# Optimization experiments

Measured on AMD Instinct MI355X. Metric: run time of the kernel, lower is better.

The kernel has to match this reference:

```python
import jax, jax.numpy as jnp
import numpy as np

N_HEAD = 2


def _time_encode(ts, freq, phase):
    # ts [N, L] -> [N, L, time_dim]; harmonic = cos(ts * basis_freq + phase)
    return jnp.cos(ts[..., None] * freq + phase)


def _layer_norm(x, g, b, eps=1e-5):
    m = jnp.mean(x, axis=-1, keepdims=True)
    v = jnp.mean((x - m) ** 2, axis=-1, keepdims=True)
    return (x - m) / jnp.sqrt(v + eps) * g + b


def _attn(src, src_t, ngh, ngh_t, mask, wq, wk, wv, fcw, fcb, lng, lnb, m1w, m1b, m2w, m2b):
    # TGAT AttnModel: src [N,h], src_t [N,1,h], ngh [N,K,h], ngh_t [N,K,h], mask [N,K] bool
    q = jnp.concatenate([src[:, None, :], src_t], axis=-1)  # [N,1,D], D=2h
    k = jnp.concatenate([ngh, ngh_t], axis=-1)              # [N,K,D]
    N, K, D = k.shape
    dk = D // N_HEAD
    qh = (q @ wq.T).reshape(N, 1, N_HEAD, dk)
    kh = (k @ wk.T).reshape(N, K, N_HEAD, dk)
    vh = (k @ wv.T).reshape(N, K, N_HEAD, dk)
    scores = jnp.einsum('nqhd,nkhd->nhqk', qh, kh) / jnp.sqrt(jnp.float32(dk))
    scores = jnp.where(mask[:, None, None, :], jnp.float32(-1e10), scores)
    a = jax.nn.softmax(scores, axis=-1)
    out = jnp.einsum('nhqk,nkhd->nqhd', a, vh).reshape(N, 1, D)
    out = out @ fcw.T + fcb
    out = _layer_norm(out + q, lng, lnb)[:, 0, :]  # residual + LN, squeeze query dim
    # MergeLayer: fc2(relu(fc1(cat[out, src])))
    h = jax.nn.relu(jnp.concatenate([out, src], axis=-1) @ m1w.T + m1b)
    return h @ m2w.T + m2b


def setup_inputs() -> dict:
    key = jax.random.key(0)
    ks = jax.random.split(key, 20)
    B, K, F, H = 2048, 20, 128, 128
    D, L, NAE, NNODE = 2 * H, 2, 4096, 100000
    s = 0.05
    n = lambda i, shape, sc=1.0: jax.random.normal(ks[i], shape, dtype=jnp.float32) * sc
    inp = {}
    inp['src_feat'] = n(0, (B, F))
    inp['src_t'] = jax.random.uniform(ks[1], (B,), jnp.float32, 0.0, 1000.0)
    inp['ngh1_idx'] = jax.random.randint(ks[2], (B, K), 0, NNODE)
    inp['ngh1_t'] = jax.random.uniform(ks[3], (B, K), jnp.float32, 0.0, 1000.0)
    inp['ngh1_feat'] = n(4, (B, K, F))
    inp['ngh2_idx'] = jax.random.randint(ks[5], (B * K, K), 0, NNODE)
    inp['ngh2_t'] = jax.random.uniform(ks[6], (B * K, K), jnp.float32, 0.0, 1000.0)
    inp['ngh2_feat'] = n(7, (B * K, K, F))
    inp['ae_x'] = n(8, (NAE, H))
    inp['ae_adj'] = jax.random.uniform(ks[9], (NAE, NAE), jnp.float32)
    inp['W_lin'] = n(10, (H, F), s)
    inp['b_lin'] = jnp.zeros((H,), jnp.float32)
    inp['basis_freq'] = (1.0 / 10 ** jnp.linspace(0.0, 9.0, H)).astype(jnp.float32)
    inp['phase'] = jnp.zeros((H,), jnp.float32)
    inp['attn_wq'] = n(11, (L, D, D), s)
    inp['attn_wk'] = n(12, (L, D, D), s)
    inp['attn_wv'] = n(13, (L, D, D), s)
    inp['attn_fc_w'] = n(14, (L, D, D), s)
    inp['attn_fc_b'] = jnp.zeros((L, D), jnp.float32)
    inp['attn_ln_g'] = jnp.ones((L, D), jnp.float32)
    inp['attn_ln_b'] = jnp.zeros((L, D), jnp.float32)
    inp['mrg_fc1_w'] = n(15, (L, H, D + H), s)
    inp['mrg_fc1_b'] = jnp.zeros((L, H), jnp.float32)
    inp['mrg_fc2_w'] = n(16, (L, H, H), s)
    inp['mrg_fc2_b'] = jnp.zeros((L, H), jnp.float32)
    inp['W_gc'] = n(17, (H, H), s)
    inp['b_gc'] = jnp.zeros((H,), jnp.float32)
    return inp


def reference(src_feat, src_t, ngh1_idx, ngh1_t, ngh1_feat, ngh2_idx, ngh2_t, ngh2_feat,
              ae_x, ae_adj, W_lin, b_lin, basis_freq, phase,
              attn_wq, attn_wk, attn_wv, attn_fc_w, attn_fc_b, attn_ln_g, attn_ln_b,
              mrg_fc1_w, mrg_fc1_b, mrg_fc2_w, mrg_fc2_b, W_gc, b_gc):
    B, K = ngh1_idx.shape
    BK = B * K
    lin = lambda x: x @ W_lin.T + b_lin
    te = lambda ts: _time_encode(ts, basis_freq, phase)
    ap = lambda i: (attn_wq[i], attn_wk[i], attn_wv[i], attn_fc_w[i], attn_fc_b[i],
                    attn_ln_g[i], attn_ln_b[i], mrg_fc1_w[i], mrg_fc1_b[i],
                    mrg_fc2_w[i], mrg_fc2_b[i])
    mask1 = ngh1_idx == 0
    mask2 = ngh2_idx == 0
    t0_B = te(jnp.zeros((B, 1), jnp.float32))
    t0_BK = te(jnp.zeros((BK, 1), jnp.float32))
    t1 = te(src_t[:, None] - ngh1_t)                         # [B,K,H]
    t2 = te(ngh1_t.reshape(BK)[:, None] - ngh2_t)            # [BK,K,H]
    # tem_conv(curr=2): layer-1 embeddings of src and its neighbors (attn layer 0)
    src_l1 = _attn(lin(src_feat), t0_B, lin(ngh1_feat), t1, mask1, *ap(0))    # [B,H]
    ngh_l1 = _attn(lin(ngh1_feat.reshape(BK, -1)), t0_BK, lin(ngh2_feat), t2, mask2, *ap(0))
    ngh_l1 = ngh_l1.reshape(B, K, -1)
    # top-level attention (attn layer 1)
    src_embed = _attn(src_l1, t0_B, ngh_l1, t1, mask1, *ap(1))                # [B,H]
    # GNN_SnapAuto autoencoder: GraphConvolution + sigmoid decode + MSE
    gc_z = ae_adj @ (ae_x @ W_gc) + b_gc
    recon_loss = jnp.mean((ae_adj - jax.nn.sigmoid(gc_z @ gc_z.T)) ** 2)
    return src_embed, recon_loss
```

## Files before the change

### kernel.cpp

```cpp
#include <hip/hip_runtime.h>
#include <math.h>


typedef _Float16 h2 __attribute__((ext_vector_type(2)));
typedef _Float16 h4 __attribute__((ext_vector_type(4)));
typedef _Float16 h8 __attribute__((ext_vector_type(8)));
typedef float f4 __attribute__((ext_vector_type(4)));


__global__ __launch_bounds__(256) void k_prep_a(
    const float* __restrict__ phase, const float* __restrict__ wq,
    const float* __restrict__ wk, const float* __restrict__ wvw,
    const float* __restrict__ Wlin, const float* __restrict__ blin,
    const float* __restrict__ m1w, const float* __restrict__ m2w,
    const float* __restrict__ Wgc,
    float* __restrict__ te0, float* __restrict__ cbf, float* __restrict__ Mb,
    float* __restrict__ OWa,
    _Float16* __restrict__ Wlinh, _Float16* __restrict__ m1wh,
    _Float16* __restrict__ m2wh, _Float16* __restrict__ WgcTh,
    float* __restrict__ lacc)
{
  __shared__ float te[128];
  __shared__ float bqv[128];
  int b = blockIdx.x, tid = threadIdx.x;

  if (b < 4) {
    int l = b >> 1, h = b & 1;
    if (tid < 128) {
      te[tid] = cosf(phase[tid]);
      if (b == 0) te0[tid] = te[tid];
    }
    __syncthreads();
    if (tid < 128) {
      const float* wr = wq + ((size_t)(l * 256 + h * 128 + tid)) * 256 + 128;
      float s = 0.f;
      for (int k = 0; k < 128; k++) s += wr[k] * te[k];
      bqv[tid] = s;
    }
    __syncthreads();
    {
      const float* wkb = wk + (size_t)l * 65536 + (size_t)h * 32768;
      float s = 0.f;
      for (int d = 0; d < 128; d++) s += wkb[(size_t)d * 256 + tid] * bqv[d];
      cbf[(l * 2 + h) * 256 + tid] = s;
    }
    return;
  }
  b -= 4;
  if (b < 512) {
    int lh = b >> 7, bx = b & 127;
    int l = lh >> 1, h = lh & 1;
    int idx = bx * 256 + tid;
    int e = idx >> 7, s = idx & 127;
    const float* wkb = wk + (size_t)l * 65536 + (size_t)h * 32768;
    const float* wqb = wq + (size_t)l * 65536 + (size_t)h * 32768;
    float acc = 0.f;
    for (int d = 0; d < 128; d++)
      acc += wkb[(size_t)d * 256 + e] * wqb[(size_t)d * 256 + s];
    Mb[(size_t)lh * 32768 + idx] = acc;
    return;
  }
  b -= 512;
  if (b < 780) {
    int ci = b / 260, bx = b % 260;
    int lyr = (ci == 2) ? 1 : 0;
    int ul  = (ci == 0) ? 1 : 0;
    float* OW = OWa + (size_t)ci * 2 * 128 * 260;
    const float* wvl = wvw + (size_t)lyr * 65536;
    int idx = bx * 256 + tid;
    int u = idx % 260; int d = (idx / 260) % 128; int h = idx / (260 * 128);
    const float* wr = wvl + (size_t)(h * 128 + d) * 256;
    float val = 0.f;
    if (u < 128) {
      if (ul) { for (int cc = 0; cc < 128; cc++) val += wr[cc] * Wlin[cc * 128 + u]; }
      else val = wr[u];
    } else if (u < 256) {
      val = wr[u];
    } else if (u == 256) {
      if (ul) { for (int cc = 0; cc < 128; cc++) val += wr[cc] * blin[cc]; }
    }
    OW[idx] = val;
    return;
  }
  b -= 780;
  {
    int idx = b * 256 + tid;
    if (idx == 0) lacc[0] = 0.f;
    int i = idx;
    if (i < 16384) { Wlinh[i] = (_Float16)Wlin[i]; return; }
    i -= 16384;
    if (i < 98304) { m1wh[i] = (_Float16)m1w[i]; return; }
    i -= 98304;
    if (i < 32768) { m2wh[i] = (_Float16)m2w[i]; return; }
    i -= 32768;
    {
      int c = i >> 7, r = i & 127;
      WgcTh[i] = (_Float16)Wgc[(size_t)r * 128 + c];
    }
  }
}


__global__ __launch_bounds__(256) void k_prep_b(
    const float* __restrict__ Mb, const float* __restrict__ cbf,
    const float* __restrict__ Wlin, const float* __restrict__ blin,
    const float* __restrict__ fcw, const float* __restrict__ OWa,
    _Float16* __restrict__ SWa, float* __restrict__ cba,
    _Float16* __restrict__ Fa)
{
  int b = blockIdx.x, tid = threadIdx.x;
  if (b < 780) {
    int ci = b / 260, bx = b % 260;
    int lyr = (ci == 2) ? 1 : 0;
    int ul  = (ci == 0) ? 1 : 0;
    const float* M2 = Mb + (size_t)lyr * 2 * 32768;
    const float* c2 = cbf + (size_t)lyr * 512;
    _Float16* SW = SWa + (size_t)ci * 520 * 128;
    float* cb = cba + (size_t)ci * 520;
    int idx = bx * 256 + tid;
    int urow = idx / 128, s = idx % 128;
    int h = urow / 260, u = urow % 260;
    const float* M = M2 + (size_t)h * 32768;
    const float* c = c2 + h * 256;
    float val = 0.f, cbv = 0.f;
    if (u < 128) {
      if (ul) {
        for (int cc = 0; cc < 128; cc++) {
          float w = Wlin[cc * 128 + u];
          val += w * M[cc * 128 + s];
          cbv += w * c[cc];
        }
      } else { val = M[u * 128 + s]; cbv = c[u]; }
    } else if (u < 256) {
      val = M[u * 128 + s]; cbv = c[u];
    } else if (u == 256) {
      if (ul) {
        for (int cc = 0; cc < 128; cc++) {
          float w = blin[cc];
          val += w * M[cc * 128 + s];
          cbv += w * c[cc];
        }
      }
    }
    SW[(size_t)urow * 128 + s] = (_Float16)val;
    if (s == 0) cb[urow] = cbv;
    return;
  }
  b -= 780;
  {
    int yy = b / 260, bx = b % 260;
    int ci = yy >> 1, h = yy & 1;
    int lyr = (ci == 2) ? 1 : 0;
    int idx = bx * 256 + tid;
    int p = idx / 260, u = idx % 260;
    const float* fw = fcw + (size_t)lyr * 65536 + (size_t)p * 256 + h * 128;
    const float* ow = OWa + (size_t)ci * 2 * 128 * 260 + (size_t)h * 128 * 260;
    float s = 0.f;
    for (int d = 0; d < 128; d++) s += fw[d] * ow[(size_t)d * 260 + u];
    Fa[(size_t)ci * 256 * 520 + (size_t)p * 520 + h * 260 + u] = (_Float16)s;
  }
}


struct GemmJob {
  const float* A; const _Float16* B; const float* bias; float* C;
  int lda, ldb, ldc, M, N, K, cmode, klen, gx, gy, nblk;
};

__device__ __forceinline__ void gemm128_body(int lb, const GemmJob& g) {
  __shared__ _Float16 As[128][72];
  __shared__ _Float16 Bs[128][72];
  int bx = lb % g.gx;
  int rest = lb / g.gx;
  int by = rest % g.gy;
  int z = rest / g.gy;

  int tid = threadIdx.x;
  int wv = tid >> 6, lane = tid & 63;
  int wm = wv >> 1, wn = wv & 1;
  int row0 = bx * 128, col0 = by * 128;
  int m0 = wm * 64, n0 = wn * 64;
  int lr = lane & 15, lk = lane >> 4;
  int kbeg = z * g.klen;
  int kend = kbeg + g.klen; if (kend > g.K) kend = g.K;

  f4 acc[4][4];
#pragma unroll
  for (int i = 0; i < 4; i++)
#pragma unroll
    for (int j = 0; j < 4; j++) acc[i][j] = (f4)0.f;

  int arow = tid >> 1;
  int acol = (tid & 1) * 32;
  int gar = row0 + arow;
  int gbr = col0 + arow;
  bool bvalid = gbr < g.N;

  for (int k0 = kbeg; k0 < kend; k0 += 64) {
    __syncthreads();
#pragma unroll
    for (int j = 0; j < 8; j++) {
      int ka = k0 + acol + j * 4;
      f4 v = (f4)0.f;
      if (ka < g.K) v = *(const f4*)&g.A[(size_t)gar * g.lda + ka];
      h4 hv = { (_Float16)v.x, (_Float16)v.y, (_Float16)v.z, (_Float16)v.w };
      *(h4*)&As[arow][acol + j * 4] = hv;
    }
#pragma unroll
    for (int j = 0; j < 8; j++) {
      int ka = k0 + acol + j * 4;
      h4 hv = (h4)(_Float16)0.f;
      if (bvalid && ka < g.K) hv = *(const h4*)&g.B[(size_t)gbr * g.ldb + ka];
      *(h4*)&Bs[arow][acol + j * 4] = hv;
    }
    __syncthreads();
#pragma unroll
    for (int kk = 0; kk < 2; kk++) {
      h8 af[4], bf[4];
#pragma unroll
      for (int i = 0; i < 4; i++)
        af[i] = *(h8*)&As[m0 + i * 16 + lr][kk * 32 + lk * 8];
#pragma unroll
      for (int j = 0; j < 4; j++)
        bf[j] = *(h8*)&Bs[n0 + j * 16 + lr][kk * 32 + lk * 8];
#pragma unroll
      for (int i = 0; i < 4; i++)
#pragma unroll
        for (int j = 0; j < 4; j++)
          acc[i][j] = __builtin_amdgcn_mfma_f32_16x16x32_f16(af[i], bf[j], acc[i][j], 0, 0, 0);
    }
  }
  float* Cz = g.C + (size_t)z * g.M * g.ldc;
#pragma unroll
  for (int j = 0; j < 4; j++) {
    int c = col0 + n0 + j * 16 + lr;
    if (c >= g.N) continue;
    float bz = (g.bias && z == 0) ? g.bias[c] : 0.f;
#pragma unroll
    for (int i = 0; i < 4; i++) {
      int rbase = row0 + m0 + i * 16 + lk * 4;
#pragma unroll
      for (int r = 0; r < 4; r++) {
        int rr = rbase + r;
        float v = acc[i][j][r] + bz;
        if (g.cmode == 0) Cz[(size_t)rr * g.ldc + c] = v;
        else if (g.cmode == 1) ((_Float16*)g.C)[(size_t)rr * g.ldc + c] = (_Float16)v;
        else ((_Float16*)g.C)[(size_t)c * g.ldc + rr] = (_Float16)v;
      }
    }
  }
}

__global__ __launch_bounds__(256) void k_gemm_multi(
    GemmJob ja, GemmJob jb, GemmJob jc, const float* lacc, float* finout)
{
  int b = blockIdx.x;
  if (b < ja.nblk) { gemm128_body(b, ja); return; }
  b -= ja.nblk;
  if (b < jb.nblk) { gemm128_body(b, jb); return; }
  b -= jb.nblk;
  if (b < jc.nblk) { gemm128_body(b, jc); return; }
  if (finout && threadIdx.x == 0)
    finout[0] = lacc[0] * (1.0f / (4096.0f * 4096.0f));
}


struct ScoreJob {
  _Float16* UY; const float* feat; const float* tsrc; const float* tngh;
  const int* idx; int rows;
};

__device__ void score_body(int row, const ScoreJob& J,
                           const float* __restrict__ freq,
                           const float* __restrict__ phase)
{
  __shared__ _Float16 fsh[20][136];
  __shared__ _Float16 tesh[20][136];
  __shared__ _Float16 ush[544];
  __shared__ float ssh[2][20];
  __shared__ float ash[2][20];
  __shared__ float dtsh[20];
  __shared__ int   msh[20];
  int tid = threadIdx.x;
  _Float16* UY = J.UY;

  if (tid < 20) {
    dtsh[tid] = J.tsrc[row] - J.tngh[(size_t)row * 20 + tid];
    msh[tid] = (J.idx[(size_t)row * 20 + tid] == 0);
  }
  if (tid < 130) {
    h4 v = *(const h4*)&UY[(size_t)row * 520 + tid * 4];
    int p4 = (tid < 65) ? tid : tid + 1;
    *(h4*)&ush[p4 * 4] = v;
  }
  const float4* fg = (const float4*)(J.feat + (size_t)row * 2560);
  for (int i = tid; i < 640; i += 256) {
    int j = i >> 5, c4 = i & 31;
    float4 v = fg[i];
    h4 hv = { (_Float16)v.x, (_Float16)v.y, (_Float16)v.z, (_Float16)v.w };
    *(h4*)&fsh[j][c4 * 4] = hv;
  }
  __syncthreads();
  for (int i = tid; i < 2560; i += 256) {
    int j = i >> 7, t = i & 127;
    tesh[j][t] = (_Float16)__cosf(dtsh[j] * freq[t] + phase[t]);
  }
  __syncthreads();

  int g = tid >> 4, li = tid & 15;
#pragma unroll
  for (int it = 0; it < 3; it++) {
    int t = it * 16 + g;
    int valid = (t < 40);
    int h = valid ? (t / 20) : 0;
    int j = valid ? (t % 20) : 0;
    float part = 0.f;
    if (valid) {
      const _Float16* xp = (li < 8) ? &fsh[j][li * 16] : &tesh[j][(li - 8) * 16];
      const _Float16* up = &ush[h * 264 + li * 16];
#pragma unroll
      for (int e = 0; e < 8; e++) {
        h2 a = *(const h2*)(xp + e * 2);
        h2 b = *(const h2*)(up + e * 2);
        part = __builtin_amdgcn_fdot2(a, b, part, false);
      }
    }
    for (int m = 8; m; m >>= 1) part += __shfl_xor(part, m, 16);
    if (valid && li == 0) ssh[h][j] = part + (float)ush[h * 264 + 256];
  }
  __syncthreads();

  if (tid < 64) {
    int head = tid >> 5, l2 = tid & 31;
    const float scale = 0.08838834764831845f;
    float s = (l2 < 20) ? (msh[l2] ? -1e10f : ssh[head][l2] * scale) : -3.0e38f;
    float mx = s;
    for (int m = 16; m; m >>= 1) mx = fmaxf(mx, __shfl_xor(mx, m, 32));
    float e = (l2 < 20) ? __expf(s - mx) : 0.f;
    float sum = e;
    for (int m = 16; m; m >>= 1) sum += __shfl_xor(sum, m, 32);
    if (l2 < 20) ash[head][l2] = e / sum;
  }
  __syncthreads();

  {
    int p = tid;
    const _Float16* colp = (p < 128) ? &fsh[0][p] : &tesh[0][p - 128];
    float a0 = 0.f, a1 = 0.f;
#pragma unroll 5
    for (int j = 0; j < 20; j++) {
      float x = (float)colp[j * 136];
      a0 += ash[0][j] * x;
      a1 += ash[1][j] * x;
    }
    UY[(size_t)row * 520 + p] = (_Float16)a0;
    UY[(size_t)row * 520 + 260 + p] = (_Float16)a1;
  }
  if (tid < 8) {
    int p = (tid < 4) ? (256 + tid) : (512 + tid);
    _Float16 v = (_Float16)((tid == 0 || tid == 4) ? 1.f : 0.f);
    UY[(size_t)row * 520 + p] = v;
  }
}

__global__ __launch_bounds__(256, 8) void k_score_multi(
    ScoreJob ja, ScoreJob jb, const float* __restrict__ freq,
    const float* __restrict__ phase,
    const float* __restrict__ zp, _Float16* __restrict__ zh, int nzb)
{
  int b = blockIdx.x;
  if (b < ja.rows) { score_body(b, ja, freq, phase); return; }
  b -= ja.rows;
  if (b < jb.rows) { score_body(b, jb, freq, phase); return; }
  b -= jb.rows;
  if (b < nzb) {
    int i = b * 256 + threadIdx.x;
    const f4* zp4 = (const f4*)zp;
    f4 s = (f4)0.f;
#pragma unroll
    for (int p = 0; p < 8; p++) {
      f4 v = zp4[(size_t)p * 131072 + i];
      s.x += v.x; s.y += v.y; s.z += v.z; s.w += v.w;
    }
    h4 o = { (_Float16)s.x, (_Float16)s.y, (_Float16)s.z, (_Float16)s.w };
    ((h4*)zh)[i] = o;
  }
}


struct TailJob {
  const _Float16* U; const _Float16* F; const float* fcb; const float* srcv;
  const float* lng; const float* lnb;
  const _Float16* m1w; const float* m1b;
  const _Float16* m2w; const float* m2b;
  float* outp; int nblk;
};

__device__ void tail_body(int blk, const TailJob& J, const float* __restrict__ te0)
{
  __shared__ _Float16 Ps[64][264];
  __shared__ _Float16 Ss[64][136];
  __shared__ float redS[64][4], redQ[64][4];
  __shared__ float mrow[64], rrow[64];
  int tid = threadIdx.x;
  int wv = tid >> 6, lane = tid & 63;
  int lr = lane & 15, lk = lane >> 4;
  int row0 = blk * 64;
  int n0 = wv * 64;

  {
    const float4* sg = (const float4*)(J.srcv + (size_t)row0 * 128);
    for (int i = tid; i < 2048; i += 256) {
      int rr = i >> 5, c4 = i & 31;
      float4 v = sg[i];
      h4 hv = { (_Float16)v.x, (_Float16)v.y, (_Float16)v.z, (_Float16)v.w };
      *(h4*)&Ss[rr][c4 * 4] = hv;
    }
  }

  f4 acc[4][4];
#pragma unroll
  for (int i = 0; i < 4; i++)
#pragma unroll
    for (int j = 0; j < 4; j++) acc[i][j] = (f4)0.f;
  for (int kt = 0; kt < 17; kt++) {
    int kb = kt * 32 + lk * 8;
    bool ok = (kb + 8 <= 520);
    h8 af[4], bf[4];
#pragma unroll
    for (int i = 0; i < 4; i++)
      af[i] = ok ? *(const h8*)&J.U[(size_t)(row0 + i * 16 + lr) * 520 + kb]
                 : (h8)(_Float16)0.f;
#pragma unroll
    for (int j = 0; j < 4; j++)
      bf[j] = ok ? *(const h8*)&J.F[(size_t)(n0 + j * 16 + lr) * 520 + kb]
                 : (h8)(_Float16)0.f;
#pragma unroll
    for (int i = 0; i < 4; i++)
#pragma unroll
      for (int j = 0; j < 4; j++)
        acc[i][j] = __builtin_amdgcn_mfma_f32_16x16x32_f16(af[i], bf[j], acc[i][j], 0, 0, 0);
  }

#pragma unroll
  for (int i = 0; i < 4; i++) {
#pragma unroll
    for (int r = 0; r < 4; r++) {
      int row_l = i * 16 + lk * 4 + r;
      float rs = 0.f, rq = 0.f;
#pragma unroll
      for (int j = 0; j < 4; j++) {
        int c = n0 + j * 16 + lr;
        float q = (c < 128) ? J.srcv[(size_t)(row0 + row_l) * 128 + c] : te0[c - 128];
        float v = acc[i][j][r] + J.fcb[c] + q;
        acc[i][j][r] = v;
        rs += v; rq += v * v;
      }
      for (int m = 8; m; m >>= 1) {
        rs += __shfl_xor(rs, m, 16);
        rq += __shfl_xor(rq, m, 16);
      }
      if (lr == 0) { redS[row_l][wv] = rs; redQ[row_l][wv] = rq; }
    }
  }
  __syncthreads();
  if (tid < 64) {
    float s4 = redS[tid][0] + redS[tid][1] + redS[tid][2] + redS[tid][3];
    float q4 = redQ[tid][0] + redQ[tid][1] + redQ[tid][2] + redQ[tid][3];
    float mean = s4 * (1.0f / 256.0f);
    float var = q4 * (1.0f / 256.0f) - mean * mean;
    mrow[tid] = mean;
    rrow[tid] = rsqrtf(var + 1e-5f);
  }
  __syncthreads();
#pragma unroll
  for (int i = 0; i < 4; i++) {
#pragma unroll
    for (int r = 0; r < 4; r++) {
      int row_l = i * 16 + lk * 4 + r;
      float mean = mrow[row_l], rstd = rrow[row_l];
#pragma unroll
      for (int j = 0; j < 4; j++) {
        int c = n0 + j * 16 + lr;
        Ps[row_l][c] = (_Float16)((acc[i][j][r] - mean) * rstd * J.lng[c] + J.lnb[c]);
      }
    }
  }
  __syncthreads();

  int wm = wv >> 1, wn = wv & 1;
  f4 a2[2][4];
#pragma unroll
  for (int i = 0; i < 2; i++)
#pragma unroll
    for (int j = 0; j < 4; j++) a2[i][j] = (f4)0.f;
  for (int kk = 0; kk < 12; kk++) {
    int kb = kk * 32 + lk * 8;
    h8 af[2], bf[4];
#pragma unroll
    for (int i = 0; i < 2; i++) {
      int rl = wm * 32 + i * 16 + lr;
      af[i] = (kb < 256) ? *(const h8*)&Ps[rl][kb] : *(const h8*)&Ss[rl][kb - 256];
    }
#pragma unroll
    for (int j = 0; j < 4; j++)
      bf[j] = *(const h8*)&J.m1w[(size_t)(wn * 64 + j * 16 + lr) * 384 + kb];
#pragma unroll
    for (int i = 0; i < 2; i++)
#pragma unroll
      for (int j = 0; j < 4; j++)
        a2[i][j] = __builtin_amdgcn_mfma_f32_16x16x32_f16(af[i], bf[j], a2[i][j], 0, 0, 0);
  }
  __syncthreads();
#pragma unroll
  for (int i = 0; i < 2; i++) {
#pragma unroll
    for (int j = 0; j < 4; j++) {
      int c = wn * 64 + j * 16 + lr;
      float bz = J.m1b[c];
#pragma unroll
      for (int r = 0; r < 4; r++) {
        float v = a2[i][j][r] + bz;
        if (v < 0.f) v = 0.f;
        Ss[wm * 32 + i * 16 + lk * 4 + r][c] = (_Float16)v;
      }
    }
  }
  __syncthreads();

  f4 a3[2][4];
#pragma unroll
  for (int i = 0; i < 2; i++)
#pragma unroll
    for (int j = 0; j < 4; j++) a3[i][j] = (f4)0.f;
#pragma unroll
  for (int kk = 0; kk < 4; kk++) {
    int kb = kk * 32 + lk * 8;
    h8 af[2], bf[4];
#pragma unroll
    for (int i = 0; i < 2; i++)
      af[i] = *(const h8*)&Ss[wm * 32 + i * 16 + lr][kb];
#pragma unroll
    for (int j = 0; j < 4; j++)
      bf[j] = *(const h8*)&J.m2w[(size_t)(wn * 64 + j * 16 + lr) * 128 + kb];
#pragma unroll
    for (int i = 0; i < 2; i++)
#pragma unroll
      for (int j = 0; j < 4; j++)
        a3[i][j] = __builtin_amdgcn_mfma_f32_16x16x32_f16(af[i], bf[j], a3[i][j], 0, 0, 0);
  }
#pragma unroll
  for (int j = 0; j < 4; j++) {
    int c = wn * 64 + j * 16 + lr;
    float bz = J.m2b[c];
#pragma unroll
    for (int i = 0; i < 2; i++) {
#pragma unroll
      for (int r = 0; r < 4; r++) {
        int rl = wm * 32 + i * 16 + lk * 4 + r;
        J.outp[(size_t)(row0 + rl) * 128 + c] = a3[i][j][r] + bz;
      }
    }
  }
}

__device__ void loss_body(int b, const _Float16* __restrict__ z,
                          const float* __restrict__ adj, float* __restrict__ acc)
{
  int bi = b & 31, bj = b >> 5;
  int tid = threadIdx.x;
  int wv = tid >> 6, lane = tid & 63;
  int wm = wv >> 1, wn = wv & 1;
  int lr = lane & 15, lk = lane >> 4;
  int row0 = bi * 128 + wm * 64;
  int col0 = bj * 128 + wn * 64;

  f4 accf[4][4];
#pragma unroll
  for (int i = 0; i < 4; i++)
#pragma unroll
    for (int j = 0; j < 4; j++) accf[i][j] = (f4)0.f;

#pragma unroll
  for (int kk = 0; kk < 4; kk++) {
    int ko = kk * 32 + lk * 8;
    h8 af[4], bf[4];
#pragma unroll
    for (int i = 0; i < 4; i++)
      af[i] = *(const h8*)&z[(size_t)(row0 + i * 16 + lr) * 128 + ko];
#pragma unroll
    for (int j = 0; j < 4; j++)
      bf[j] = *(const h8*)&z[(size_t)(col0 + j * 16 + lr) * 128 + ko];
#pragma unroll
    for (int i = 0; i < 4; i++)
#pragma unroll
      for (int j = 0; j < 4; j++)
        accf[i][j] = __builtin_amdgcn_mfma_f32_16x16x32_f16(af[i], bf[j], accf[i][j], 0, 0, 0);
  }

  float lsum = 0.f;
#pragma unroll
  for (int i = 0; i < 4; i++) {
    int rbase = row0 + i * 16 + lk * 4;
#pragma unroll
    for (int r = 0; r < 4; r++) {
      const float* arow = adj + (size_t)(rbase + r) * 4096;
#pragma unroll
      for (int j = 0; j < 4; j++) {
        float x = accf[i][j][r];
        float s = 1.0f / (1.0f + __expf(-x));
        float d = arow[col0 + j * 16 + lr] - s;
        lsum += d * d;
      }
    }
  }
  for (int m = 32; m; m >>= 1) lsum += __shfl_xor(lsum, m, 64);
  if (lane == 0) atomicAdd(acc, lsum);
}

__global__ __launch_bounds__(256) void k_tail_loss(
    TailJob ja, TailJob jb, const float* __restrict__ te0,
    const _Float16* __restrict__ z, const float* __restrict__ adj,
    float* __restrict__ lacc, int nloss)
{
  int b = blockIdx.x;
  if (b < ja.nblk) { tail_body(b, ja, te0); return; }
  b -= ja.nblk;
  if (b < jb.nblk) { tail_body(b, jb, te0); return; }
  b -= jb.nblk;
  if (b < nloss) loss_body(b, z, adj, lacc);
}


extern "C" void kernel_launch(void* const* d_in, const int* in_sizes, int n_in,
                              void* d_out, int out_size, void* d_ws, size_t ws_size,
                              hipStream_t stream) {
  const float* src_feat  = (const float*)d_in[0];
  const float* src_t     = (const float*)d_in[1];
  const int*   ngh1_idx  = (const int*)d_in[2];
  const float* ngh1_t    = (const float*)d_in[3];
  const float* ngh1_feat = (const float*)d_in[4];
  const int*   ngh2_idx  = (const int*)d_in[5];
  const float* ngh2_t    = (const float*)d_in[6];
  const float* ngh2_feat = (const float*)d_in[7];
  const float* ae_x      = (const float*)d_in[8];
  const float* ae_adj    = (const float*)d_in[9];
  const float* W_lin     = (const float*)d_in[10];
  const float* b_lin     = (const float*)d_in[11];
  const float* freq      = (const float*)d_in[12];
  const float* phase     = (const float*)d_in[13];
  const float* wq        = (const float*)d_in[14];
  const float* wk        = (const float*)d_in[15];
  const float* wvp       = (const float*)d_in[16];
  const float* fcw       = (const float*)d_in[17];
  const float* fcb       = (const float*)d_in[18];
  const float* lng       = (const float*)d_in[19];
  const float* lnb       = (const float*)d_in[20];
  const float* m1w       = (const float*)d_in[21];
  const float* m1b       = (const float*)d_in[22];
  const float* m2w       = (const float*)d_in[23];
  const float* m2b       = (const float*)d_in[24];
  const float* W_gc      = (const float*)d_in[25];
  const float* b_gc      = (const float*)d_in[26];
  float* out = (float*)d_out;

  const int NB = 2048, NA = 40960;

  char* w = (char*)d_ws;
  size_t off = 0;
  auto alloc = [&](size_t bytes) -> void* {
    void* p = (void*)(w + off);
    off += (bytes + 255) & ~(size_t)255;
    return p;
  };
  float* te0    = (float*)alloc(128 * 4);
  float* linS   = (float*)alloc((size_t)NB * 128 * 4);
  float* lin1   = (float*)alloc((size_t)NA * 128 * 4);
  float* src_l1 = (float*)alloc((size_t)NB * 128 * 4);
  float* ngh_l1 = (float*)alloc((size_t)NA * 128 * 4);
  float* Mb     = (float*)alloc((size_t)4 * 32768 * 4);
  float* cbf    = (float*)alloc(4 * 256 * 4);
  _Float16* SWh = (_Float16*)alloc((size_t)3 * 520 * 128 * 2);
  float* cbU    = (float*)alloc(3 * 520 * 4);
  float* OW     = (float*)alloc((size_t)3 * 2 * 128 * 260 * 4);
  _Float16* Fh  = (_Float16*)alloc((size_t)3 * 256 * 520 * 2);
  _Float16* Wlinh = (_Float16*)alloc(16384 * 2);
  _Float16* m1wh  = (_Float16*)alloc((size_t)2 * 128 * 384 * 2);
  _Float16* m2wh  = (_Float16*)alloc((size_t)2 * 128 * 128 * 2);
  _Float16* WgcTh = (_Float16*)alloc(16384 * 2);
  _Float16* xwTh  = (_Float16*)alloc((size_t)4096 * 128 * 2);
  float* zpart    = (float*)alloc((size_t)8 * 4096 * 128 * 4);
  _Float16* zh    = (_Float16*)alloc((size_t)4096 * 128 * 2);
  float* lacc     = (float*)alloc(256);
  _Float16* UbufA = (_Float16*)alloc((size_t)NA * 520 * 2);
  _Float16* UbufB = (_Float16*)alloc((size_t)NB * 520 * 2);
  _Float16* UbufC = (_Float16*)alloc((size_t)NB * 520 * 2);

  k_prep_a<<<1936, 256, 0, stream>>>(phase, wq, wk, wvp, W_lin, b_lin, m1w, m2w,
                                     W_gc, te0, cbf, Mb, OW, Wlinh, m1wh, m2wh,
                                     WgcTh, lacc);
  k_prep_b<<<2340, 256, 0, stream>>>(Mb, cbf, W_lin, b_lin, fcw, OW, SWh, cbU, Fh);

  GemmJob j0 = {};

  GemmJob jLinS = { src_feat,  Wlinh, b_lin,   linS,         128, 128, 128,
                    2048, 128, 128, 0, 128, 16, 1, 16 };
  GemmJob jLin1 = { ngh1_feat, Wlinh, b_lin,   lin1,         128, 128, 128,
                    40960, 128, 128, 0, 128, 320, 1, 320 };
  GemmJob jXwT  = { ae_x,      WgcTh, nullptr, (float*)xwTh, 128, 128, 4096,
                    4096, 128, 128, 2, 128, 32, 1, 32 };
  k_gemm_multi<<<368, 256, 0, stream>>>(jLinS, jLin1, jXwT, nullptr, nullptr);

  GemmJob jUA = { lin1, SWh,              cbU,       (float*)UbufA, 128, 128, 520,
                  40960, 520, 128, 1, 128, 320, 5, 1600 };
  GemmJob jUB = { linS, SWh + 520 * 128,  cbU + 520, (float*)UbufB, 128, 128, 520,
                  2048, 520, 128, 1, 128, 16, 5, 80 };
  GemmJob jZB = { ae_adj, xwTh, b_gc, zpart, 4096, 4096, 128,
                  4096, 128, 4096, 0, 512, 32, 1, 256 };
  k_gemm_multi<<<1936, 256, 0, stream>>>(jUA, jUB, jZB, nullptr, nullptr);

  ScoreJob sA = { UbufA, ngh2_feat, ngh1_t, ngh2_t, ngh2_idx, NA };
  ScoreJob sB = { UbufB, lin1,      src_t,  ngh1_t, ngh1_idx, NB };
  k_score_multi<<<NA + NB + 512, 256, 0, stream>>>(sA, sB, freq, phase,
                                                   zpart, zh, 512);

  TailJob tA = { UbufA, Fh,             fcb, lin1, lng, lnb,
                 m1wh, m1b, m2wh, m2b, ngh_l1, NA / 64 };
  TailJob tB = { UbufB, Fh + 256 * 520, fcb, linS, lng, lnb,
                 m1wh, m1b, m2wh, m2b, src_l1, NB / 64 };
  k_tail_loss<<<NA / 64 + NB / 64 + 1024, 256, 0, stream>>>(
      tA, tB, te0, zh, ae_adj, lacc, 1024);

  GemmJob jUC = { src_l1, SWh + 2 * 520 * 128, cbU + 2 * 520, (float*)UbufC,
                  128, 128, 520, 2048, 520, 128, 1, 128, 16, 5, 80 };
  k_gemm_multi<<<81, 256, 0, stream>>>(jUC, j0, j0, lacc, out + (size_t)NB * 128);

  ScoreJob sC = { UbufC, ngh_l1, src_t, ngh1_t, ngh1_idx, NB };
  ScoreJob s0 = {};
  k_score_multi<<<NB, 256, 0, stream>>>(sC, s0, freq, phase, nullptr, nullptr, 0);

  TailJob tC = { UbufC, Fh + 2 * 256 * 520, fcb + 256, src_l1, lng + 256, lnb + 256,
                 m1wh + 128 * 384, m1b + 128, m2wh + 128 * 128, m2b + 128,
                 out, NB / 64 };
  TailJob t0 = {};
  k_tail_loss<<<NB / 64, 256, 0, stream>>>(tC, t0, te0, nullptr, nullptr,
                                           nullptr, 0);
}
```

Before: 502.1 us.

## Fuse top-level attention stage into one kernel and merge first GEMMs into prep

The three final launches for the top-level attention (U projection GEMM, score/softmax/aggregation, and the fc+LayerNorm+merge MLP tail) are replaced by a single kernel. Each of its 32 blocks handles 64 rows end to end and keeps intermediates in shared memory, so the UbufC round trip and two launch gaps go away. The lin/xwT GEMM jobs are also folded into the k_prep_b launch to drop one more launch. The trade-off is that the fused kernel runs only 32 blocks, one per CU, which may leave most of the GPU idle during that stage.

```diff
diff --git a/kernel.cpp b/kernel.cpp
--- a/kernel.cpp
+++ b/kernel.cpp
@@ -101,12 +101,103 @@
 }
 
 
+struct GemmJob {
+  const float* A; const _Float16* B; const float* bias; float* C;
+  int lda, ldb, ldc, M, N, K, cmode, klen, gx, gy, nblk;
+};
+
+__device__ __forceinline__ void gemm128_body(int lb, const GemmJob& g) {
+  __shared__ _Float16 As[128][72];
+  __shared__ _Float16 Bs[128][72];
+  int bx = lb % g.gx;
+  int rest = lb / g.gx;
+  int by = rest % g.gy;
+  int z = rest / g.gy;
+
+  int tid = threadIdx.x;
+  int wv = tid >> 6, lane = tid & 63;
+  int wm = wv >> 1, wn = wv & 1;
+  int row0 = bx * 128, col0 = by * 128;
+  int m0 = wm * 64, n0 = wn * 64;
+  int lr = lane & 15, lk = lane >> 4;
+  int kbeg = z * g.klen;
+  int kend = kbeg + g.klen; if (kend > g.K) kend = g.K;
+
+  f4 acc[4][4];
+#pragma unroll
+  for (int i = 0; i < 4; i++)
+#pragma unroll
+    for (int j = 0; j < 4; j++) acc[i][j] = (f4)0.f;
+
+  int arow = tid >> 1;
+  int acol = (tid & 1) * 32;
+  int gar = row0 + arow;
+  int gbr = col0 + arow;
+  bool bvalid = gbr < g.N;
+
+  for (int k0 = kbeg; k0 < kend; k0 += 64) {
+    __syncthreads();
+#pragma unroll
+    for (int j = 0; j < 8; j++) {
+      int ka = k0 + acol + j * 4;
+      f4 v = (f4)0.f;
+      if (ka < g.K) v = *(const f4*)&g.A[(size_t)gar * g.lda + ka];
+      h4 hv = { (_Float16)v.x, (_Float16)v.y, (_Float16)v.z, (_Float16)v.w };
+      *(h4*)&As[arow][acol + j * 4] = hv;
+    }
+#pragma unroll
+    for (int j = 0; j < 8; j++) {
+      int ka = k0 + acol + j * 4;
+      h4 hv = (h4)(_Float16)0.f;
+      if (bvalid && ka < g.K) hv = *(const h4*)&g.B[(size_t)gbr * g.ldb + ka];
+      *(h4*)&Bs[arow][acol + j * 4] = hv;
+    }
+    __syncthreads();
+#pragma unroll
+    for (int kk = 0; kk < 2; kk++) {
+      h8 af[4], bf[4];
+#pragma unroll
+      for (int i = 0; i < 4; i++)
+        af[i] = *(h8*)&As[m0 + i * 16 + lr][kk * 32 + lk * 8];
+#pragma unroll
+      for (int j = 0; j < 4; j++)
+        bf[j] = *(h8*)&Bs[n0 + j * 16 + lr][kk * 32 + lk * 8];
+#pragma unroll
+      for (int i = 0; i < 4; i++)
+#pragma unroll
+        for (int j = 0; j < 4; j++)
+          acc[i][j] = __builtin_amdgcn_mfma_f32_16x16x32_f16(af[i], bf[j], acc[i][j], 0, 0, 0);
+    }
+  }
+  float* Cz = g.C + (size_t)z * g.M * g.ldc;
+#pragma unroll
+  for (int j = 0; j < 4; j++) {
+    int c = col0 + n0 + j * 16 + lr;
+    if (c >= g.N) continue;
+    float bz = (g.bias && z == 0) ? g.bias[c] : 0.f;
+#pragma unroll
+    for (int i = 0; i < 4; i++) {
+      int rbase = row0 + m0 + i * 16 + lk * 4;
+#pragma unroll
+      for (int r = 0; r < 4; r++) {
+        int rr = rbase + r;
+        float v = acc[i][j][r] + bz;
+        if (g.cmode == 0) Cz[(size_t)rr * g.ldc + c] = v;
+        else if (g.cmode == 1) ((_Float16*)g.C)[(size_t)rr * g.ldc + c] = (_Float16)v;
+        else ((_Float16*)g.C)[(size_t)c * g.ldc + rr] = (_Float16)v;
+      }
+    }
+  }
+}
+
+
 __global__ __launch_bounds__(256) void k_prep_b(
     const float* __restrict__ Mb, const float* __restrict__ cbf,
     const float* __restrict__ Wlin, const float* __restrict__ blin,
     const float* __restrict__ fcw, const float* __restrict__ OWa,
     _Float16* __restrict__ SWa, float* __restrict__ cba,
-    _Float16* __restrict__ Fa)
+    _Float16* __restrict__ Fa,
+    GemmJob j1, GemmJob j2, GemmJob j3)
 {
   int b = blockIdx.x, tid = threadIdx.x;
   if (b < 780) {
@@ -147,7 +238,7 @@
     return;
   }
   b -= 780;
-  {
+  if (b < 1560) {
     int yy = b / 260, bx = b % 260;
     int ci = yy >> 1, h = yy & 1;
     int lyr = (ci == 2) ? 1 : 0;
@@ -158,101 +249,18 @@
     float s = 0.f;
     for (int d = 0; d < 128; d++) s += fw[d] * ow[(size_t)d * 260 + u];
     Fa[(size_t)ci * 256 * 520 + (size_t)p * 520 + h * 260 + u] = (_Float16)s;
-  }
+    return;
+  }
+  b -= 1560;
+  if (b < j1.nblk) { gemm128_body(b, j1); return; }
+  b -= j1.nblk;
+  if (b < j2.nblk) { gemm128_body(b, j2); return; }
+  b -= j2.nblk;
+  if (b < j3.nblk) { gemm128_body(b, j3); return; }
 }
 
-
-struct GemmJob {
-  const float* A; const _Float16* B; const float* bias; float* C;
-  int lda, ldb, ldc, M, N, K, cmode, klen, gx, gy, nblk;
-};
-
-__device__ __forceinline__ void gemm128_body(int lb, const GemmJob& g) {
-  __shared__ _Float16 As[128][72];
-  __shared__ _Float16 Bs[128][72];
-  int bx = lb % g.gx;
-  int rest = lb / g.gx;
-  int by = rest % g.gy;
-  int z = rest / g.gy;
-
-  int tid = threadIdx.x;
-  int wv = tid >> 6, lane = tid & 63;
-  int wm = wv >> 1, wn = wv & 1;
-  int row0 = bx * 128, col0 = by * 128;
-  int m0 = wm * 64, n0 = wn * 64;
-  int lr = lane & 15, lk = lane >> 4;
-  int kbeg = z * g.klen;
-  int kend = kbeg + g.klen; if (kend > g.K) kend = g.K;
-
-  f4 acc[4][4];
-#pragma unroll
-  for (int i = 0; i < 4; i++)
-#pragma unroll
-    for (int j = 0; j < 4; j++) acc[i][j] = (f4)0.f;
-
-  int arow = tid >> 1;
-  int acol = (tid & 1) * 32;
-  int gar = row0 + arow;
-  int gbr = col0 + arow;
-  bool bvalid = gbr < g.N;
-
-  for (int k0 = kbeg; k0 < kend; k0 += 64) {
-    __syncthreads();
-#pragma unroll
-    for (int j = 0; j < 8; j++) {
-      int ka = k0 + acol + j * 4;
-      f4 v = (f4)0.f;
-      if (ka < g.K) v = *(const f4*)&g.A[(size_t)gar * g.lda + ka];
-      h4 hv = { (_Float16)v.x, (_Float16)v.y, (_Float16)v.z, (_Float16)v.w };
-      *(h4*)&As[arow][acol + j * 4] = hv;
-    }
-#pragma unroll
-    for (int j = 0; j < 8; j++) {
-      int ka = k0 + acol + j * 4;
-      h4 hv = (h4)(_Float16)0.f;
-      if (bvalid && ka < g.K) hv = *(const h4*)&g.B[(size_t)gbr * g.ldb + ka];
-      *(h4*)&Bs[arow][acol + j * 4] = hv;
-    }
-    __syncthreads();
-#pragma unroll
-    for (int kk = 0; kk < 2; kk++) {
-      h8 af[4], bf[4];
-#pragma unroll
-      for (int i = 0; i < 4; i++)
-        af[i] = *(h8*)&As[m0 + i * 16 + lr][kk * 32 + lk * 8];
-#pragma unroll
-      for (int j = 0; j < 4; j++)
-        bf[j] = *(h8*)&Bs[n0 + j * 16 + lr][kk * 32 + lk * 8];
-#pragma unroll
-      for (int i = 0; i < 4; i++)
-#pragma unroll
-        for (int j = 0; j < 4; j++)
-          acc[i][j] = __builtin_amdgcn_mfma_f32_16x16x32_f16(af[i], bf[j], acc[i][j], 0, 0, 0);
-    }
-  }
-  float* Cz = g.C + (size_t)z * g.M * g.ldc;
-#pragma unroll
-  for (int j = 0; j < 4; j++) {
-    int c = col0 + n0 + j * 16 + lr;
-    if (c >= g.N) continue;
-    float bz = (g.bias && z == 0) ? g.bias[c] : 0.f;
-#pragma unroll
-    for (int i = 0; i < 4; i++) {
-      int rbase = row0 + m0 + i * 16 + lk * 4;
-#pragma unroll
-      for (int r = 0; r < 4; r++) {
-        int rr = rbase + r;
-        float v = acc[i][j][r] + bz;
-        if (g.cmode == 0) Cz[(size_t)rr * g.ldc + c] = v;
-        else if (g.cmode == 1) ((_Float16*)g.C)[(size_t)rr * g.ldc + c] = (_Float16)v;
-        else ((_Float16*)g.C)[(size_t)c * g.ldc + rr] = (_Float16)v;
-      }
-    }
-  }
-}
-
 __global__ __launch_bounds__(256) void k_gemm_multi(
-    GemmJob ja, GemmJob jb, GemmJob jc, const float* lacc, float* finout)
+    GemmJob ja, GemmJob jb, GemmJob jc)
 {
   int b = blockIdx.x;
   if (b < ja.nblk) { gemm128_body(b, ja); return; }
@@ -260,8 +268,6 @@
   if (b < jb.nblk) { gemm128_body(b, jb); return; }
   b -= jb.nblk;
   if (b < jc.nblk) { gemm128_body(b, jc); return; }
-  if (finout && threadIdx.x == 0)
-    finout[0] = lacc[0] * (1.0f / (4096.0f * 4096.0f));
 }
 
 
@@ -321,8 +327,8 @@
 #pragma unroll
       for (int e = 0; e < 8; e++) {
         h2 a = *(const h2*)(xp + e * 2);
-        h2 b = *(const h2*)(up + e * 2);
-        part = __builtin_amdgcn_fdot2(a, b, part, false);
+        h2 b2 = *(const h2*)(up + e * 2);
+        part = __builtin_amdgcn_fdot2(a, b2, part, false);
       }
     }
     for (int m = 8; m; m >>= 1) part += __shfl_xor(part, m, 16);
@@ -629,6 +635,333 @@
   if (b < jb.nblk) { tail_body(b, jb, te0); return; }
   b -= jb.nblk;
   if (b < nloss) loss_body(b, z, adj, lacc);
+}
+
+
+__global__ __launch_bounds__(256, 1) void k_callC(
+    const float* __restrict__ src_l1,
+    const _Float16* __restrict__ SWc,
+    const float* __restrict__ cbc,
+    const float* __restrict__ featp,
+    const float* __restrict__ tsrc, const float* __restrict__ tngh,
+    const int* __restrict__ idxp,
+    const float* __restrict__ freq, const float* __restrict__ phase,
+    const _Float16* __restrict__ F,
+    const float* __restrict__ fcb, const float* __restrict__ lng,
+    const float* __restrict__ lnb,
+    const _Float16* __restrict__ m1w, const float* __restrict__ m1b,
+    const _Float16* __restrict__ m2w, const float* __restrict__ m2b,
+    const float* __restrict__ te0,
+    float* __restrict__ outp, const float* __restrict__ lacc,
+    float* __restrict__ finout)
+{
+  __shared__ _Float16 Uls[64][536];
+  __shared__ __align__(16) _Float16 Scr[4][5440];
+  __shared__ _Float16 Ssh[64][136];
+  __shared__ float redS[64][4], redQ[64][4];
+  __shared__ float mrow[64], rrow[64];
+  __shared__ float sshA[4][2][20], ashA[4][2][20], dtA[4][20];
+  __shared__ int   mskA[4][20];
+  __shared__ float fqs[128], phs[128];
+
+  int tid = threadIdx.x;
+  int wv = tid >> 6, lane = tid & 63;
+  int lr = lane & 15, lk = lane >> 4;
+  int row0 = blockIdx.x * 64;
+
+  if (blockIdx.x == 0 && tid == 0)
+    finout[0] = lacc[0] * (1.0f / (4096.0f * 4096.0f));
+  if (tid < 128) { fqs[tid] = freq[tid]; phs[tid] = phase[tid]; }
+
+  {
+    const float4* sg = (const float4*)(src_l1 + (size_t)row0 * 128);
+    for (int i = tid; i < 2048; i += 256) {
+      int rr = i >> 5, c4 = i & 31;
+      float4 v = sg[i];
+      h4 hv = { (_Float16)v.x, (_Float16)v.y, (_Float16)v.z, (_Float16)v.w };
+      *(h4*)&Ssh[rr][c4 * 4] = hv;
+    }
+  }
+  __syncthreads();
+
+  {
+    f4 acc[4][9];
+#pragma unroll
+    for (int i = 0; i < 4; i++)
+#pragma unroll
+      for (int j = 0; j < 9; j++) acc[i][j] = (f4)0.f;
+#pragma unroll
+    for (int kt = 0; kt < 4; kt++) {
+      int kb = kt * 32 + lk * 8;
+      h8 af[4];
+#pragma unroll
+      for (int rf = 0; rf < 4; rf++)
+        af[rf] = *(const h8*)&Ssh[rf * 16 + lr][kb];
+#pragma unroll
+      for (int ci = 0; ci < 9; ci++) {
+        int cf = wv + ci * 4;
+        if (cf < 33) {
+          int srow = cf * 16 + lr;
+          h8 bf = (srow < 520) ? *(const h8*)&SWc[(size_t)srow * 128 + kb]
+                               : (h8)(_Float16)0.f;
+#pragma unroll
+          for (int rf = 0; rf < 4; rf++)
+            acc[rf][ci] = __builtin_amdgcn_mfma_f32_16x16x32_f16(af[rf], bf, acc[rf][ci], 0, 0, 0);
+        }
+      }
+    }
+#pragma unroll
+    for (int ci = 0; ci < 9; ci++) {
+      int cf = wv + ci * 4;
+      if (cf < 33) {
+        int c = cf * 16 + lr;
+        if (c < 520) {
+          float bz = cbc[c];
+#pragma unroll
+          for (int rf = 0; rf < 4; rf++)
+#pragma unroll
+            for (int r = 0; r < 4; r++)
+              Uls[rf * 16 + lk * 4 + r][c] = (_Float16)(acc[rf][ci][r] + bz);
+        }
+      }
+    }
+  }
+  __syncthreads();
+
+  {
+    _Float16* fsh = &Scr[wv][0];
+    _Float16* tesh = &Scr[wv][2720];
+    for (int t = 0; t < 16; t++) {
+      int row_l = wv * 16 + t;
+      int grow = row0 + row_l;
+      if (lane < 20) {
+        dtA[wv][lane] = tsrc[grow] - tngh[(size_t)grow * 20 + lane];
+        mskA[wv][lane] = (idxp[(size_t)grow * 20 + lane] == 0);
+      }
+      const float4* fg = (const float4*)(featp + (size_t)grow * 2560);
+      for (int i = lane; i < 640; i += 64) {
+        int j = i >> 5, c4 = i & 31;
+        float4 v = fg[i];
+        h4 hv = { (_Float16)v.x, (_Float16)v.y, (_Float16)v.z, (_Float16)v.w };
+        *(h4*)&fsh[j * 136 + c4 * 4] = hv;
+      }
+      __builtin_amdgcn_wave_barrier();
+      for (int i = lane; i < 2560; i += 64) {
+        int j = i >> 7, tt = i & 127;
+        tesh[j * 136 + tt] = (_Float16)__cosf(dtA[wv][j] * fqs[tt] + phs[tt]);
+      }
+      __builtin_amdgcn_wave_barrier();
+      {
+        int g2 = lane >> 4, li = lane & 15;
+#pragma unroll
+        for (int it = 0; it < 10; it++) {
+          int t40 = it * 4 + g2;
+          int h = t40 / 20, j = t40 % 20;
+          const _Float16* xp = (li < 8) ? &fsh[j * 136 + li * 16]
+                                        : &tesh[j * 136 + (li - 8) * 16];
+          const _Float16* up = &Uls[row_l][h * 260 + li * 16];
+          float part = 0.f;
+#pragma unroll
+          for (int e = 0; e < 8; e++) {
+            h2 a = *(const h2*)(xp + e * 2);
+            h2 b2 = *(const h2*)(up + e * 2);
+            part = __builtin_amdgcn_fdot2(a, b2, part, false);
+          }
+          for (int m = 8; m; m >>= 1) part += __shfl_xor(part, m, 16);
+          if (li == 0) sshA[wv][h][j] = part + (float)Uls[row_l][h * 260 + 256];
+        }
+      }
+      __builtin_amdgcn_wave_barrier();
+      {
+        int head = lane >> 5, l2 = lane & 31;
+        const float scale = 0.08838834764831845f;
+        float s = (l2 < 20) ? (mskA[wv][l2] ? -1e10f : sshA[wv][head][l2] * scale)
+                            : -3.0e38f;
+        float mx = s;
+        for (int m = 16; m; m >>= 1) mx = fmaxf(mx, __shfl_xor(mx, m, 32));
+        float e = (l2 < 20) ? __expf(s - mx) : 0.f;
+        float sum = e;
+        for (int m = 16; m; m >>= 1) sum += __shfl_xor(sum, m, 32);
+        if (l2 < 20) ashA[wv][head][l2] = e / sum;
+      }
+      __builtin_amdgcn_wave_barrier();
+      {
+        int c0 = lane * 4;
+        float a0[4] = {0.f, 0.f, 0.f, 0.f}, a1[4] = {0.f, 0.f, 0.f, 0.f};
+#pragma unroll 5
+        for (int j = 0; j < 20; j++) {
+          float w0 = ashA[wv][0][j], w1 = ashA[wv][1][j];
+          h4 x = (c0 < 128) ? *(const h4*)&fsh[j * 136 + c0]
+                            : *(const h4*)&tesh[j * 136 + (c0 - 128)];
+#pragma unroll
+          for (int e = 0; e < 4; e++) {
+            float xf = (float)x[e];
+            a0[e] += w0 * xf; a1[e] += w1 * xf;
+          }
+        }
+        h4 o0 = { (_Float16)a0[0], (_Float16)a0[1], (_Float16)a0[2], (_Float16)a0[3] };
+        h4 o1 = { (_Float16)a1[0], (_Float16)a1[1], (_Float16)a1[2], (_Float16)a1[3] };
+        *(h4*)&Uls[row_l][c0] = o0;
+        *(h4*)&Uls[row_l][260 + c0] = o1;
+        if (lane == 0) {
+          h4 pad = { (_Float16)1.f, (_Float16)0.f, (_Float16)0.f, (_Float16)0.f };
+          *(h4*)&Uls[row_l][256] = pad;
+          *(h4*)&Uls[row_l][516] = pad;
+        }
+      }
+      __builtin_amdgcn_wave_barrier();
+    }
+  }
+  __syncthreads();
+
+  _Float16 (*Ps)[264] = (_Float16(*)[264])&Scr[0][0];
+  int n0 = wv * 64;
+  {
+    f4 acc[4][4];
+#pragma unroll
+    for (int i = 0; i < 4; i++)
+#pragma unroll
+      for (int j = 0; j < 4; j++) acc[i][j] = (f4)0.f;
+    for (int kt = 0; kt < 17; kt++) {
+      int kb = kt * 32 + lk * 8;
+      bool ok = (kb + 8 <= 520);
+      h8 af[4], bf[4];
+#pragma unroll
+      for (int i = 0; i < 4; i++)
+        af[i] = ok ? *(const h8*)&Uls[i * 16 + lr][kb] : (h8)(_Float16)0.f;
+#pragma unroll
+      for (int j = 0; j < 4; j++)
+        bf[j] = ok ? *(const h8*)&F[(size_t)(n0 + j * 16 + lr) * 520 + kb]
+                   : (h8)(_Float16)0.f;
+#pragma unroll
+      for (int i = 0; i < 4; i++)
+#pragma unroll
+        for (int j = 0; j < 4; j++)
+          acc[i][j] = __builtin_amdgcn_mfma_f32_16x16x32_f16(af[i], bf[j], acc[i][j], 0, 0, 0);
+    }
+#pragma unroll
+    for (int i = 0; i < 4; i++) {
+#pragma unroll
+      for (int r = 0; r < 4; r++) {
+        int row_l = i * 16 + lk * 4 + r;
+        float rs = 0.f, rq = 0.f;
+#pragma unroll
+        for (int j = 0; j < 4; j++) {
+          int c = n0 + j * 16 + lr;
+          float q = (c < 128) ? src_l1[(size_t)(row0 + row_l) * 128 + c] : te0[c - 128];
+          float v = acc[i][j][r] + fcb[c] + q;
+          acc[i][j][r] = v;
+          rs += v; rq += v * v;
+        }
+        for (int m = 8; m; m >>= 1) {
+          rs += __shfl_xor(rs, m, 16);
+          rq += __shfl_xor(rq, m, 16);
+        }
+        if (lr == 0) { redS[row_l][wv] = rs; redQ[row_l][wv] = rq; }
+      }
+    }
+    __syncthreads();
+    if (tid < 64) {
+      float s4 = redS[tid][0] + redS[tid][1] + redS[tid][2] + redS[tid][3];
+      float q4 = redQ[tid][0] + redQ[tid][1] + redQ[tid][2] + redQ[tid][3];
+      float mean = s4 * (1.0f / 256.0f);
+      float var = q4 * (1.0f / 256.0f) - mean * mean;
+      mrow[tid] = mean;
+      rrow[tid] = rsqrtf(var + 1e-5f);
+    }
+    __syncthreads();
+#pragma unroll
+    for (int i = 0; i < 4; i++) {
+#pragma unroll
+      for (int r = 0; r < 4; r++) {
+        int row_l = i * 16 + lk * 4 + r;
+        float mean = mrow[row_l], rstd = rrow[row_l];
+#pragma unroll
+        for (int j = 0; j < 4; j++) {
+          int c = n0 + j * 16 + lr;
+          Ps[row_l][c] = (_Float16)((acc[i][j][r] - mean) * rstd * lng[c] + lnb[c]);
+        }
+      }
+    }
+    __syncthreads();
+  }
+  int wm = wv >> 1, wn = wv & 1;
+  {
+    f4 a2[2][4];
+#pragma unroll
+    for (int i = 0; i < 2; i++)
+#pragma unroll
+      for (int j = 0; j < 4; j++) a2[i][j] = (f4)0.f;
+    for (int kk = 0; kk < 12; kk++) {
+      int kb = kk * 32 + lk * 8;
+      h8 af[2], bf[4];
+#pragma unroll
+      for (int i = 0; i < 2; i++) {
+        int rl = wm * 32 + i * 16 + lr;
+        af[i] = (kb < 256) ? *(const h8*)&Ps[rl][kb] : *(const h8*)&Ssh[rl][kb - 256];
+      }
+#pragma unroll
+      for (int j = 0; j < 4; j++)
+        bf[j] = *(const h8*)&m1w[(size_t)(wn * 64 + j * 16 + lr) * 384 + kb];
+#pragma unroll
+      for (int i = 0; i < 2; i++)
+#pragma unroll
+        for (int j = 0; j < 4; j++)
+          a2[i][j] = __builtin_amdgcn_mfma_f32_16x16x32_f16(af[i], bf[j], a2[i][j], 0, 0, 0);
+    }
+    __syncthreads();
+#pragma unroll
+    for (int i = 0; i < 2; i++) {
+#pragma unroll
+      for (int j = 0; j < 4; j++) {
+        int c = wn * 64 + j * 16 + lr;
+        float bz = m1b[c];
+#pragma unroll
+        for (int r = 0; r < 4; r++) {
+          float v = a2[i][j][r] + bz;
+          if (v < 0.f) v = 0.f;
+          Ssh[wm * 32 + i * 16 + lk * 4 + r][c] = (_Float16)v;
+        }
+      }
+    }
+    __syncthreads();
+  }
+  {
+    f4 a3[2][4];
+#pragma unroll
+    for (int i = 0; i < 2; i++)
+#pragma unroll
+      for (int j = 0; j < 4; j++) a3[i][j] = (f4)0.f;
+#pragma unroll
+    for (int kk = 0; kk < 4; kk++) {
+      int kb = kk * 32 + lk * 8;
+      h8 af[2], bf[4];
+#pragma unroll
+      for (int i = 0; i < 2; i++)
+        af[i] = *(const h8*)&Ssh[wm * 32 + i * 16 + lr][kb];
+#pragma unroll
+      for (int j = 0; j < 4; j++)
+        bf[j] = *(const h8*)&m2w[(size_t)(wn * 64 + j * 16 + lr) * 128 + kb];
+#pragma unroll
+      for (int i = 0; i < 2; i++)
+#pragma unroll
+        for (int j = 0; j < 4; j++)
+          a3[i][j] = __builtin_amdgcn_mfma_f32_16x16x32_f16(af[i], bf[j], a3[i][j], 0, 0, 0);
+    }
+#pragma unroll
+    for (int j = 0; j < 4; j++) {
+      int c = wn * 64 + j * 16 + lr;
+      float bz = m2b[c];
+#pragma unroll
+      for (int i = 0; i < 2; i++) {
+#pragma unroll
+        for (int r = 0; r < 4; r++) {
+          int rl = wm * 32 + i * 16 + lk * 4 + r;
+          outp[(size_t)(row0 + rl) * 128 + c] = a3[i][j][r] + bz;
+        }
+      }
+    }
+  }
 }
 
 
@@ -694,14 +1027,10 @@
   float* lacc     = (float*)alloc(256);
   _Float16* UbufA = (_Float16*)alloc((size_t)NA * 520 * 2);
   _Float16* UbufB = (_Float16*)alloc((size_t)NB * 520 * 2);
-  _Float16* UbufC = (_Float16*)alloc((size_t)NB * 520 * 2);
 
   k_prep_a<<<1936, 256, 0, stream>>>(phase, wq, wk, wvp, W_lin, b_lin, m1w, m2w,
                                      W_gc, te0, cbf, Mb, OW, Wlinh, m1wh, m2wh,
                                      WgcTh, lacc);
-  k_prep_b<<<2340, 256, 0, stream>>>(Mb, cbf, W_lin, b_lin, fcw, OW, SWh, cbU, Fh);
-
-  GemmJob j0 = {};
 
   GemmJob jLinS = { src_feat,  Wlinh, b_lin,   linS,         128, 128, 128,
                     2048, 128, 128, 0, 128, 16, 1, 16 };
@@ -709,7 +1038,8 @@
                     40960, 128, 128, 0, 128, 320, 1, 320 };
   GemmJob jXwT  = { ae_x,      WgcTh, nullptr, (float*)xwTh, 128, 128, 4096,
                     4096, 128, 128, 2, 128, 32, 1, 32 };
-  k_gemm_multi<<<368, 256, 0, stream>>>(jLinS, jLin1, jXwT, nullptr, nullptr);
+  k_prep_b<<<2708, 256, 0, stream>>>(Mb, cbf, W_lin, b_lin, fcw, OW, SWh, cbU,
+                                     Fh, jLinS, jLin1, jXwT);
 
   GemmJob jUA = { lin1, SWh,              cbU,       (float*)UbufA, 128, 128, 520,
                   40960, 520, 128, 1, 128, 320, 5, 1600 };
@@ -717,7 +1047,7 @@
                   2048, 520, 128, 1, 128, 16, 5, 80 };
   GemmJob jZB = { ae_adj, xwTh, b_gc, zpart, 4096, 4096, 128,
                   4096, 128, 4096, 0, 512, 32, 1, 256 };
-  k_gemm_multi<<<1936, 256, 0, stream>>>(jUA, jUB, jZB, nullptr, nullptr);
+  k_gemm_multi<<<1936, 256, 0, stream>>>(jUA, jUB, jZB);
 
   ScoreJob sA = { UbufA, ngh2_feat, ngh1_t, ngh2_t, ngh2_idx, NA };
   ScoreJob sB = { UbufB, lin1,      src_t,  ngh1_t, ngh1_idx, NB };
@@ -731,18 +1061,9 @@
   k_tail_loss<<<NA / 64 + NB / 64 + 1024, 256, 0, stream>>>(
       tA, tB, te0, zh, ae_adj, lacc, 1024);
 
-  GemmJob jUC = { src_l1, SWh + 2 * 520 * 128, cbU + 2 * 520, (float*)UbufC,
-                  128, 128, 520, 2048, 520, 128, 1, 128, 16, 5, 80 };
-  k_gemm_multi<<<81, 256, 0, stream>>>(jUC, j0, j0, lacc, out + (size_t)NB * 128);
-
-  ScoreJob sC = { UbufC, ngh_l1, src_t, ngh1_t, ngh1_idx, NB };
-  ScoreJob s0 = {};
-  k_score_multi<<<NB, 256, 0, stream>>>(sC, s0, freq, phase, nullptr, nullptr, 0);
-
-  TailJob tC = { UbufC, Fh + 2 * 256 * 520, fcb + 256, src_l1, lng + 256, lnb + 256,
-                 m1wh + 128 * 384, m1b + 128, m2wh + 128 * 128, m2b + 128,
-                 out, NB / 64 };
-  TailJob t0 = {};
-  k_tail_loss<<<NB / 64, 256, 0, stream>>>(tC, t0, te0, nullptr, nullptr,
-                                           nullptr, 0);
+  k_callC<<<32, 256, 0, stream>>>(
+      src_l1, SWh + 2 * 520 * 128, cbU + 2 * 520, ngh_l1, src_t, ngh1_t,
+      ngh1_idx, freq, phase, Fh + 2 * 256 * 520, fcb + 256, lng + 256, lnb + 256,
+      m1wh + 128 * 384, m1b + 128, m2wh + 128 * 128, m2b + 128, te0,
+      out, lacc, out + (size_t)NB * 128);
 }
```

Measured after the change: 641.4 us. 1.28x slower.
